# Kernel tuning notes

Measured on AMD Instinct MI355X. Metric: run time of the kernel, lower is better.

The kernel has to match this reference:

```python
import jax, jax.numpy as jnp
import numpy as np

B, T, C, H = 2, 2048, 1024, 16
DH = C // H  # head_size = 64
EPS = 1e-5


def layernorm_axis1(x, gamma, beta):
    # Faithful to the torch code: mean/var over dim 1 (TIME axis), unbiased var.
    mean = jnp.mean(x, axis=1, keepdims=True)
    var = jnp.var(x, axis=1, ddof=1, keepdims=True)
    xhat = (x - mean) / jnp.sqrt(var + EPS)
    return gamma * xhat + beta


def setup_inputs() -> dict:
    key = jax.random.key(0)
    ks = jax.random.split(key, 16)
    s_in = 1.0 / np.sqrt(C)
    s_cat = 1.0 / np.sqrt(H * DH)
    s_ff = 1.0 / np.sqrt(4 * C)
    return {
        "x": jax.random.normal(ks[0], (B, T, C), dtype=jnp.float32),
        # per-head Q/K/V projections (no bias), stacked: [H, C, DH]
        "Wq": jax.random.uniform(ks[1], (H, C, DH), jnp.float32, -s_in, s_in),
        "Wk": jax.random.uniform(ks[2], (H, C, DH), jnp.float32, -s_in, s_in),
        "Wv": jax.random.uniform(ks[3], (H, C, DH), jnp.float32, -s_in, s_in),
        # attention output projection [H*DH, C] + bias
        "Wo": jax.random.uniform(ks[4], (H * DH, C), jnp.float32, -s_cat, s_cat),
        "bo": jax.random.uniform(ks[5], (C,), jnp.float32, -s_cat, s_cat),
        # FFN
        "W1": jax.random.uniform(ks[6], (C, 4 * C), jnp.float32, -s_in, s_in),
        "b1": jax.random.uniform(ks[7], (4 * C,), jnp.float32, -s_in, s_in),
        "W2": jax.random.uniform(ks[8], (4 * C, C), jnp.float32, -s_ff, s_ff),
        "b2": jax.random.uniform(ks[9], (C,), jnp.float32, -s_ff, s_ff),
        # LayerNorm affine params (plain tensors in the original)
        "gamma1": jnp.ones((C,), jnp.float32),
        "beta1": jnp.zeros((C,), jnp.float32),
        "gamma2": jnp.ones((C,), jnp.float32),
        "beta2": jnp.zeros((C,), jnp.float32),
    }


def reference(x, Wq, Wk, Wv, Wo, bo, W1, b1, W2, b2, gamma1, beta1, gamma2, beta2):
    # --- pre-LN attention sublayer ---
    x1 = layernorm_axis1(x, gamma1, beta1)                     # [B,T,C]
    q = jnp.einsum("btc,hcd->bhtd", x1, Wq)                    # [B,H,T,DH]
    k = jnp.einsum("btc,hcd->bhtd", x1, Wk)
    v = jnp.einsum("btc,hcd->bhtd", x1, Wv)
    # NOTE: scaled by full embedding dim C (not head_size) — faithful to source.
    scores = jnp.einsum("bhtd,bhsd->bhts", q, k) * (C ** -0.5)  # [B,H,T,T]
    causal = jnp.tril(jnp.ones((T, T), dtype=bool))
    scores = jnp.where(causal, scores, -jnp.inf)
    wei = jax.nn.softmax(scores, axis=-1)
    attn = jnp.einsum("bhts,bhsd->bhtd", wei, v)               # [B,H,T,DH]
    attn = attn.transpose(0, 2, 1, 3).reshape(B, T, H * DH)    # concat heads
    x = x + attn @ Wo + bo
    # --- pre-LN FFN sublayer ---
    x2 = layernorm_axis1(x, gamma2, beta2)
    h = jax.nn.relu(x2 @ W1 + b1)
    x = x + h @ W2 + b2
    return x
```

## Files before the change

kernel.cpp:

```cpp
#include <hip/hip_runtime.h>
#include <math.h>


#define TDIM 2048
#define BDIM 2
#define CDIM 1024
#define HDIM 16
#define DHE  64
#define QKVS 3072
#define NT   32
#define LNEPS 1e-5f
#define SC2  0.0450842200278f

typedef float f32x4 __attribute__((ext_vector_type(4)));
typedef __bf16 bf16x8 __attribute__((ext_vector_type(8)));
typedef __bf16 bf16x4 __attribute__((ext_vector_type(4)));

__device__ __forceinline__ void gld_lds16(const __bf16* g, __bf16* l) {
  __builtin_amdgcn_global_load_lds(
      (const __attribute__((address_space(1))) void*)g,
      (__attribute__((address_space(3))) void*)l, 16, 0, 0);
}

__global__ __launch_bounds__(256) void ln_stats(const float* __restrict__ x,
                                                float* __restrict__ sumv,
                                                float* __restrict__ sqv) {
  int c = blockIdx.x * 256 + threadIdx.x;
  int b = blockIdx.y;
  int t0 = blockIdx.z * (TDIM / 16);
  const float* xp = x + ((size_t)b * TDIM + t0) * CDIM + c;
  float s = 0.f, q = 0.f;
  for (int t = 0; t < TDIM / 16; ++t) {
    float v = xp[(size_t)t * CDIM];
    s += v;
    q += v * v;
  }
  atomicAdd(&sumv[b * CDIM + c], s);
  atomicAdd(&sqv[b * CDIM + c], q);
}

__global__ __launch_bounds__(256) void ln_apply(const float* __restrict__ x,
    const float* __restrict__ sumv, const float* __restrict__ sqv,
    const float* __restrict__ gamma, const float* __restrict__ beta,
    __bf16* __restrict__ y) {
  size_t i = (size_t)blockIdx.x * 256 + threadIdx.x;
  int c = (int)(i & (CDIM - 1));
  int b = (int)(i >> 21);
  float mean = sumv[b * CDIM + c] * (1.f / TDIM);
  float var = (sqv[b * CDIM + c] - mean * mean * (float)TDIM) * (1.f / (TDIM - 1));
  float rstd = rsqrtf(var + LNEPS);
  y[i] = (__bf16)(gamma[c] * (x[i] - mean) * rstd + beta[c]);
}

__global__ __launch_bounds__(256) void pack_all(
    const float* __restrict__ Wq, const float* __restrict__ Wk,
    const float* __restrict__ Wv, const float* __restrict__ Wo,
    const float* __restrict__ W1, const float* __restrict__ W2,
    __bf16* __restrict__ Wqkvb, __bf16* __restrict__ Wob,
    __bf16* __restrict__ W1b, __bf16* __restrict__ W2b) {
  __shared__ float tile[32][33];
  int t = blockIdx.x;
  int tx = threadIdx.x & 31, ty = threadIdx.x >> 5;
  if (t < 3072) {
    int mat = t >> 10, rem = t & 1023;
    int h = rem >> 6, rr = rem & 63;
    int c0 = (rr & 31) * 32, d0 = (rr >> 5) * 32;
    const float* W = (mat == 0) ? Wq : (mat == 1) ? Wk : Wv;
#pragma unroll
    for (int i = 0; i < 4; ++i)
      tile[ty + i * 8][tx] = W[((size_t)h * CDIM + c0 + ty + i * 8) * DHE + d0 + tx];
    __syncthreads();
#pragma unroll
    for (int i = 0; i < 4; ++i) {
      int n = mat * 1024 + h * 64 + d0 + ty + i * 8;
      Wqkvb[(size_t)n * CDIM + c0 + tx] = (__bf16)tile[tx][ty + i * 8];
    }
  } else {
    const float* in; __bf16* outp; int Cc, R, l;
    if (t < 4096)      { in = Wo; outp = Wob; R = 1024; Cc = 1024; l = t - 3072; }
    else if (t < 8192) { in = W1; outp = W1b; R = 1024; Cc = 4096; l = t - 4096; }
    else               { in = W2; outp = W2b; R = 4096; Cc = 1024; l = t - 8192; }
    int ncx = Cc >> 5;
    int c0 = (l % ncx) * 32, r0 = (l / ncx) * 32;
#pragma unroll
    for (int i = 0; i < 4; ++i)
      tile[ty + i * 8][tx] = in[(size_t)(r0 + ty + i * 8) * Cc + c0 + tx];
    __syncthreads();
#pragma unroll
    for (int i = 0; i < 4; ++i)
      outp[(size_t)(c0 + ty + i * 8) * R + r0 + tx] = (__bf16)tile[tx][ty + i * 8];
  }
}

__global__ __launch_bounds__(256) void transp_v(const __bf16* __restrict__ qkv,
    __bf16* __restrict__ vtb) {
  __shared__ __bf16 tile[32][33];
  int bh = blockIdx.y >> 1, d0 = (blockIdx.y & 1) * 32;
  int b = bh >> 4, h = bh & 15;
  int t0 = blockIdx.x * 32;
  int tx = threadIdx.x & 31, ty = threadIdx.x >> 5;
#pragma unroll
  for (int i = 0; i < 4; ++i)
    tile[ty + i * 8][tx] = qkv[((size_t)b * TDIM + t0 + ty + i * 8) * QKVS + 2048 + h * DHE + d0 + tx];
  __syncthreads();
#pragma unroll
  for (int i = 0; i < 4; ++i)
    vtb[((size_t)bh * 64 + d0 + ty + i * 8) * TDIM + t0 + tx] = tile[tx][ty + i * 8];
}

template<bool BIAS, bool RES, bool RELU, bool OUTBF>
__global__ __launch_bounds__(256) void gemm_bf16(
    const __bf16* __restrict__ Ag, const __bf16* __restrict__ Bg,
    const float* __restrict__ bias, const float* __restrict__ res,
    void* __restrict__ Cm, int M, int N, int K) {
  __shared__ __bf16 As[128 * 32];
  __shared__ __bf16 Bs[128 * 32];
  int tid = threadIdx.x;
  int lane = tid & 63, wid = tid >> 6;
  int wr = wid >> 1, wc = wid & 1;
  int m0 = blockIdx.y * 128, n0 = blockIdx.x * 128;
  int srow = tid >> 2, scol = (tid & 3) * 8;
  int l15 = lane & 15, k8 = (lane >> 4) * 8;

  f32x4 acc[4][4];
#pragma unroll
  for (int m = 0; m < 4; ++m)
#pragma unroll
    for (int n = 0; n < 4; ++n) acc[m][n] = (f32x4){0.f, 0.f, 0.f, 0.f};

  for (int k0 = 0; k0 < K; k0 += 32) {
    __syncthreads();
    gld_lds16(Ag + (size_t)(m0 + srow) * K + k0 + scol,       As + tid * 8);
    gld_lds16(Ag + (size_t)(m0 + 64 + srow) * K + k0 + scol,  As + 2048 + tid * 8);
    gld_lds16(Bg + (size_t)(n0 + srow) * K + k0 + scol,       Bs + tid * 8);
    gld_lds16(Bg + (size_t)(n0 + 64 + srow) * K + k0 + scol,  Bs + 2048 + tid * 8);
    __syncthreads();

    bf16x8 af[4], bf[4];
#pragma unroll
    for (int m = 0; m < 4; ++m)
      af[m] = *(const bf16x8*)(As + (wr * 64 + m * 16 + l15) * 32 + k8);
#pragma unroll
    for (int n = 0; n < 4; ++n)
      bf[n] = *(const bf16x8*)(Bs + (wc * 64 + n * 16 + l15) * 32 + k8);
#pragma unroll
    for (int m = 0; m < 4; ++m)
#pragma unroll
      for (int n = 0; n < 4; ++n)
        acc[m][n] = __builtin_amdgcn_mfma_f32_16x16x32_bf16(af[m], bf[n], acc[m][n], 0, 0, 0);
  }

  int rbase = (lane >> 4) * 4;
#pragma unroll
  for (int m = 0; m < 4; ++m) {
    int row = m0 + wr * 64 + m * 16 + rbase;
#pragma unroll
    for (int n = 0; n < 4; ++n) {
      int col = n0 + wc * 64 + n * 16 + l15;
#pragma unroll
      for (int j = 0; j < 4; ++j) {
        float v = acc[m][n][j];
        size_t off = (size_t)(row + j) * N + col;
        if (BIAS) v += bias[col];
        if (RES)  v += res[off];
        if (RELU) v = fmaxf(v, 0.f);
        if (OUTBF) ((__bf16*)Cm)[off] = (__bf16)v;
        else       ((float*)Cm)[off] = v;
      }
    }
  }
}

template<bool BIAS, bool RELU, bool OUTBF>
__global__ __launch_bounds__(512, 2) void gemm256(
    const __bf16* __restrict__ Ag, const __bf16* __restrict__ Bg,
    const float* __restrict__ bias, void* __restrict__ Cm, void* __restrict__ Cm2,
    int M, int N, int K, int ld, int gnx) {
  __shared__ __align__(16) char lds[131072];
  int tid = threadIdx.x;
  int lane = tid & 63, wid = tid >> 6;
  int wm = wid >> 2, wn = wid & 3;
  int l15 = lane & 15, hi = lane >> 4;

  size_t koff = (size_t)blockIdx.y * K;
  Ag += koff; Bg += koff;
  void* Cuse = blockIdx.y ? Cm2 : Cm;

  int nwg = gridDim.x;
  int q = nwg >> 3, r = nwg & 7;
  int xcd = blockIdx.x & 7, pos = blockIdx.x >> 3;
  int wgid = (xcd < r ? xcd * (q + 1) : r * (q + 1) + (xcd - r) * q) + pos;
  int m0 = (wgid / gnx) * 256, n0 = (wgid % gnx) * 256;

  int sr = tid >> 3;
  int skcol = ((tid & 7) ^ (sr & 7)) << 3;

  const int ac0 = (hi * 16) ^ ((l15 & 7) << 4);
  const int ac1 = ac0 ^ 64;

  f32x4 acc[8][4];
#pragma unroll
  for (int i = 0; i < 8; ++i)
#pragma unroll
    for (int j = 0; j < 4; ++j) acc[i][j] = (f32x4){0.f, 0.f, 0.f, 0.f};

  auto stage = [&](const __bf16* __restrict__ G, int grow0, int k0, char* dst) {
#pragma unroll
    for (int c = 0; c < 2; ++c)
      gld_lds16(G + (size_t)(grow0 + c * 64 + sr) * ld + k0 + skcol,
                (__bf16*)(dst + c * 8192) + (size_t)tid * 8);
  };

  int KT = K >> 6;
  stage(Ag, m0,       0, lds);
  stage(Ag, m0 + 128, 0, lds + 16384);
  stage(Bg, n0,       0, lds + 32768);
  stage(Bg, n0 + 128, 0, lds + 32768 + 16384);
  asm volatile("s_waitcnt vmcnt(0)" ::: "memory");
  __builtin_amdgcn_s_barrier();

  bf16x8 a[4][2], b[4][2];

#define LOADA(MH) do { \
    const char* Ac_ = lds + (size_t)cur * 65536; \
    int rb_ = (wm * 128 + (MH) * 64 + l15) * 128; \
    _Pragma("unroll") \
    for (int i_ = 0; i_ < 4; ++i_) { \
      a[i_][0] = *(const bf16x8*)(Ac_ + rb_ + i_ * 2048 + ac0); \
      a[i_][1] = *(const bf16x8*)(Ac_ + rb_ + i_ * 2048 + ac1); \
    } } while (0)
#define LOADBF do { \
    const char* Bc_ = lds + (size_t)cur * 65536 + 32768; \
    int rb_ = (wn * 64 + l15) * 128; \
    _Pragma("unroll") \
    for (int j_ = 0; j_ < 4; ++j_) { \
      b[j_][0] = *(const bf16x8*)(Bc_ + rb_ + j_ * 2048 + ac0); \
      b[j_][1] = *(const bf16x8*)(Bc_ + rb_ + j_ * 2048 + ac1); \
    } } while (0)
#define QUAD(MH, NH) do { \
    _Pragma("unroll") \
    for (int i_ = 0; i_ < 4; ++i_) \
    _Pragma("unroll") \
    for (int j_ = 0; j_ < 2; ++j_) { \
      acc[(MH)*4+i_][(NH)*2+j_] = __builtin_amdgcn_mfma_f32_16x16x32_bf16( \
          a[i_][0], b[(NH)*2+j_][0], acc[(MH)*4+i_][(NH)*2+j_], 0, 0, 0); \
      acc[(MH)*4+i_][(NH)*2+j_] = __builtin_amdgcn_mfma_f32_16x16x32_bf16( \
          a[i_][1], b[(NH)*2+j_][1], acc[(MH)*4+i_][(NH)*2+j_], 0, 0, 0); \
    } } while (0)

  for (int kt = 0; kt < KT; ++kt) {
    int cur = kt & 1;
    char* Lnxt = lds + (size_t)(cur ^ 1) * 65536;
    int k1 = (kt + 1) << 6;
    if (kt < KT - 1) {
      stage(Ag, m0,       k1, Lnxt);
      stage(Ag, m0 + 128, k1, Lnxt + 16384);
      stage(Bg, n0,       k1, Lnxt + 32768);
      stage(Bg, n0 + 128, k1, Lnxt + 32768 + 16384);
    }
    LOADBF;
    LOADA(0);
    __builtin_amdgcn_s_setprio(1);
    QUAD(0, 0); QUAD(0, 1);
    __builtin_amdgcn_s_setprio(0);
    LOADA(1);
    __builtin_amdgcn_s_setprio(1);
    QUAD(1, 0); QUAD(1, 1);
    __builtin_amdgcn_s_setprio(0);
    asm volatile("" ::: "memory");
    asm volatile("s_waitcnt vmcnt(0)" ::: "memory");
    __builtin_amdgcn_s_barrier();
  }
#undef LOADA
#undef LOADBF
#undef QUAD

#pragma unroll
  for (int fm = 0; fm < 8; ++fm) {
    int row = m0 + wm * 128 + fm * 16 + hi * 4;
#pragma unroll
    for (int fn = 0; fn < 4; ++fn) {
      int col = n0 + wn * 64 + fn * 16 + l15;
#pragma unroll
      for (int j = 0; j < 4; ++j) {
        float v = acc[fm][fn][j];
        size_t off = (size_t)(row + j) * N + col;
        if (BIAS) v += bias[col];
        if (RELU) v = fmaxf(v, 0.f);
        if (OUTBF) ((__bf16*)Cuse)[off] = (__bf16)v;
        else       ((float*)Cuse)[off] = v;
      }
    }
  }
}

__global__ __launch_bounds__(256) void ffn2_reduce(const float* __restrict__ p0,
    const float* __restrict__ p1, const float* __restrict__ b2,
    const float* __restrict__ xmid, float* __restrict__ out) {
  size_t i = ((size_t)blockIdx.x * 256 + threadIdx.x) * 4;
  int c = (int)(i & (CDIM - 1));
  float4 a = *(const float4*)(p0 + i);
  float4 b = *(const float4*)(p1 + i);
  float4 r = *(const float4*)(xmid + i);
  float4 bb = *(const float4*)(b2 + c);
  float4 v;
  v.x = a.x + b.x + r.x + bb.x;
  v.y = a.y + b.y + r.y + bb.y;
  v.z = a.z + b.z + r.z + bb.z;
  v.w = a.w + b.w + r.w + bb.w;
  *(float4*)(out + i) = v;
}

__global__ __launch_bounds__(512, 4) void attn_mfma(const __bf16* __restrict__ qkv,
    const __bf16* __restrict__ vt, __bf16* __restrict__ o) {
  __shared__ __align__(16) char smem[55296];
  __bf16 (*Ks)[64][72] = (__bf16 (*)[64][72])(smem);
  __bf16 (*Vs)[64][72] = (__bf16 (*)[64][72])(smem + 18432);
  __bf16 (*Ps)[16][72] = (__bf16 (*)[16][72])(smem + 36864);
  float (*Os)[64]      = (float (*)[64])(smem);
  float* ms = (float*)(smem + 16384);
  float* ls = (float*)(smem + 16640);

  int bh = blockIdx.y;
  int b = bh >> 4, h = bh & 15;
  int bxA = blockIdx.x;
  int bxB = NT - 1 - bxA;
  int tid = threadIdx.x;
  int lane = tid & 63, w = tid >> 6;
  int wq = w & 3;
  int g = w >> 2;
  int l15 = lane & 15, hi = lane >> 4;
  int hi4 = hi * 4;
  size_t bT = (size_t)b * TDIM;

  bf16x8 onesb;
#pragma unroll
  for (int i = 0; i < 8; ++i) onesb[i] = (l15 == 0) ? (__bf16)1.0f : (__bf16)0.0f;

  bf16x8 qfA[2], qfB[2];
  {
    const __bf16* qp = qkv + (bT + bxA * 64 + wq * 16 + l15) * QKVS + h * DHE;
    qfA[0] = *(const bf16x8*)(qp + hi * 8);
    qfA[1] = *(const bf16x8*)(qp + 32 + hi * 8);
    qp = qkv + (bT + bxB * 64 + wq * 16 + l15) * QKVS + h * DHE;
    qfB[0] = *(const bf16x8*)(qp + hi * 8);
    qfB[1] = *(const bf16x8*)(qp + 32 + hi * 8);
  }

  float mA = -INFINITY, mB = -INFINITY;
  f32x4 lA = (f32x4){0.f, 0.f, 0.f, 0.f};
  f32x4 lB = (f32x4){0.f, 0.f, 0.f, 0.f};
  f32x4 oA[4], oB[4];
#pragma unroll
  for (int n = 0; n < 4; ++n) {
    oA[n] = (f32x4){0.f, 0.f, 0.f, 0.f};
    oB[n] = (f32x4){0.f, 0.f, 0.f, 0.f};
  }

  int g_tid = tid & 255;
  int r0 = g_tid >> 3, c8 = (g_tid & 7) * 8;

  auto process = [&](const bf16x8* qf, float& m_i, f32x4& l_acc, f32x4* oacc,
                     int bx, int t2) {
    f32x4 sacc[4];
#pragma unroll
    for (int n = 0; n < 4; ++n) sacc[n] = (f32x4){0.f, 0.f, 0.f, 0.f};
    __builtin_amdgcn_s_setprio(1);
#pragma unroll
    for (int n = 0; n < 4; ++n)
#pragma unroll
      for (int kk = 0; kk < 2; ++kk) {
        bf16x8 kf = *(const bf16x8*)&Ks[g][n * 16 + l15][kk * 32 + hi * 8];
        sacc[n] = __builtin_amdgcn_mfma_f32_16x16x32_bf16(kf, qf[kk], sacc[n], 0, 0, 0);
      }
    __builtin_amdgcn_s_setprio(0);

    int myq = wq * 16 + l15;
    if (t2 == bx) {
#pragma unroll
      for (int n = 0; n < 4; ++n)
#pragma unroll
        for (int j = 0; j < 4; ++j)
          if (n * 16 + hi4 + j > myq) sacc[n][j] = -INFINITY;
    }

    float mx = sacc[0][0];
#pragma unroll
    for (int n = 0; n < 4; ++n) {
      float a0 = fmaxf(sacc[n][0], sacc[n][1]);
      float a1 = fmaxf(sacc[n][2], sacc[n][3]);
      mx = fmaxf(mx, fmaxf(a0, a1));
    }
    mx = fmaxf(mx, __shfl_xor(mx, 16));
    mx = fmaxf(mx, __shfl_xor(mx, 32));
    mx *= SC2;

    if (!__all(mx - m_i <= 8.0f)) {
      float nm = fmaxf(m_i, mx);
      float al = exp2f(m_i - nm);
      m_i = nm;
#pragma unroll
      for (int r = 0; r < 4; ++r) {
        float ao = __shfl(al, hi4 + r);
        l_acc[r] *= ao;
#pragma unroll
        for (int n = 0; n < 4; ++n) oacc[n][r] *= ao;
      }
    }

    float negm = -m_i;
#pragma unroll
    for (int n = 0; n < 4; ++n) {
      bf16x4 pv;
#pragma unroll
      for (int j = 0; j < 4; ++j)
        pv[j] = (__bf16)exp2f(fmaf(sacc[n][j], SC2, negm));
      *(bf16x4*)&Ps[w][l15][n * 16 + hi4] = pv;
    }

    bf16x8 pa0 = *(const bf16x8*)&Ps[w][l15][hi * 8];
    bf16x8 pa1 = *(const bf16x8*)&Ps[w][l15][32 + hi * 8];
    __builtin_amdgcn_s_setprio(1);
#pragma unroll
    for (int n = 0; n < 4; ++n) {
      bf16x8 vf0 = *(const bf16x8*)&Vs[g][n * 16 + l15][hi * 8];
      bf16x8 vf1 = *(const bf16x8*)&Vs[g][n * 16 + l15][32 + hi * 8];
      oacc[n] = __builtin_amdgcn_mfma_f32_16x16x32_bf16(pa0, vf0, oacc[n], 0, 0, 0);
      oacc[n] = __builtin_amdgcn_mfma_f32_16x16x32_bf16(pa1, vf1, oacc[n], 0, 0, 0);
    }
    l_acc = __builtin_amdgcn_mfma_f32_16x16x32_bf16(pa0, onesb, l_acc, 0, 0, 0);
    l_acc = __builtin_amdgcn_mfma_f32_16x16x32_bf16(pa1, onesb, l_acc, 0, 0, 0);
    __builtin_amdgcn_s_setprio(0);
  };

  for (int j = 0; j <= bxB / 2; ++j) {
    int t2 = 2 * j + g;
    bool have = (t2 <= bxB);
    __syncthreads();
    if (have) {
#pragma unroll
      for (int rr = 0; rr < 2; ++rr) {
        int row = rr * 32 + r0;
        *(bf16x8*)&Ks[g][row][c8] =
            *(const bf16x8*)(qkv + (bT + t2 * 64 + row) * QKVS + 1024 + h * DHE + c8);
        *(bf16x8*)&Vs[g][row][c8] =
            *(const bf16x8*)(vt + ((size_t)bh * 64 + row) * TDIM + t2 * 64 + c8);
      }
    }
    __syncthreads();
    if (t2 <= bxA) process(qfA, mA, lA, oA, bxA, t2);
    if (have)      process(qfB, mB, lB, oB, bxB, t2);
  }

  auto merge = [&](int bx, float m_i, const f32x4& l_acc, f32x4* oacc) {
    float m_o[4], l_o[4];
#pragma unroll
    for (int r = 0; r < 4; ++r) {
      m_o[r] = __shfl(m_i, hi4 + r);
      l_o[r] = __shfl(l_acc[r], lane & 48);
    }
    __syncthreads();
    if (g == 1) {
#pragma unroll
      for (int r = 0; r < 4; ++r) {
        int lrow = wq * 16 + hi4 + r;
        if (l15 == 0) { ms[lrow] = m_o[r]; ls[lrow] = l_o[r]; }
#pragma unroll
        for (int n = 0; n < 4; ++n)
          Os[lrow][n * 16 + l15] = oacc[n][r];
      }
    }
    __syncthreads();
    if (g == 0) {
#pragma unroll
      for (int r = 0; r < 4; ++r) {
        int lrow = wq * 16 + hi4 + r;
        float m1 = ms[lrow], l1 = ls[lrow];
        float mm = fmaxf(m_o[r], m1);
        float e0 = exp2f(m_o[r] - mm), e1 = exp2f(m1 - mm);
        float inv = 1.f / (l_o[r] * e0 + l1 * e1);
        size_t row = bT + bx * 64 + lrow;
#pragma unroll
        for (int n = 0; n < 4; ++n) {
          float v = (oacc[n][r] * e0 + Os[lrow][n * 16 + l15] * e1) * inv;
          o[row * CDIM + h * DHE + n * 16 + l15] = (__bf16)v;
        }
      }
    }
  };
  merge(bxA, mA, lA, oA);
  merge(bxB, mB, lB, oB);
}

extern "C" void kernel_launch(void* const* d_in, const int* in_sizes, int n_in,
                              void* d_out, int out_size, void* d_ws, size_t ws_size,
                              hipStream_t stream) {
  (void)in_sizes; (void)n_in; (void)out_size; (void)ws_size;
  const float* x   = (const float*)d_in[0];
  const float* Wq  = (const float*)d_in[1];
  const float* Wk  = (const float*)d_in[2];
  const float* Wv  = (const float*)d_in[3];
  const float* Wo  = (const float*)d_in[4];
  const float* bo  = (const float*)d_in[5];
  const float* W1  = (const float*)d_in[6];
  const float* b1  = (const float*)d_in[7];
  const float* W2  = (const float*)d_in[8];
  const float* b2  = (const float*)d_in[9];
  const float* g1  = (const float*)d_in[10];
  const float* be1 = (const float*)d_in[11];
  const float* g2  = (const float*)d_in[12];
  const float* be2 = (const float*)d_in[13];
  float* out = (float*)d_out;

  char* wsb = (char*)d_ws;
  const size_t MB = 1024 * 1024;
  __bf16* Wqkvb = (__bf16*)(wsb + 0);
  __bf16* Wob   = (__bf16*)(wsb + 6  * MB);
  __bf16* W1b   = (__bf16*)(wsb + 8  * MB);
  __bf16* W2b   = (__bf16*)(wsb + 16 * MB);
  __bf16* qkvb  = (__bf16*)(wsb + 24 * MB);
  __bf16* hb    = (__bf16*)(wsb + 24 * MB);
  __bf16* vtb   = (__bf16*)(wsb + 48 * MB);
  __bf16* x1b   = (__bf16*)(wsb + 56 * MB);
  __bf16* attnb = (__bf16*)(wsb + 56 * MB);
  float*  xmid  = (float*) (wsb + 64 * MB);
  __bf16* x2b   = (__bf16*)(wsb + 80 * MB);
  float*  stats = (float*) (wsb + 88 * MB);
  float*  p0    = (float*) (wsb + 0);
  float*  p1    = (float*) (wsb + 48 * MB);
  float* sum1 = stats,        *sq1 = stats + 2048;
  float* sum2 = stats + 4096, *sq2 = stats + 6144;

  hipMemsetAsync(stats, 0, 4 * 2048 * sizeof(float), stream);

  pack_all<<<dim3(12288), 256, 0, stream>>>(Wq, Wk, Wv, Wo, W1, W2,
                                            Wqkvb, Wob, W1b, W2b);

  ln_stats<<<dim3(CDIM / 256, BDIM, 16), 256, 0, stream>>>(x, sum1, sq1);
  ln_apply<<<dim3((BDIM * TDIM * CDIM) / 256), 256, 0, stream>>>(x, sum1, sq1, g1, be1, x1b);

  gemm256<false, false, true><<<dim3(192, 1), 512, 0, stream>>>(
      x1b, Wqkvb, nullptr, qkvb, qkvb, 4096, 3072, 1024, 1024, 12);

  transp_v<<<dim3(TDIM / 32, 64), 256, 0, stream>>>(qkvb, vtb);

  attn_mfma<<<dim3(NT / 2, BDIM * HDIM), 512, 0, stream>>>(qkvb, vtb, attnb);

  gemm_bf16<true, true, false, false><<<dim3(8, 32), 256, 0, stream>>>(
      attnb, Wob, bo, x, xmid, 4096, 1024, 1024);

  ln_stats<<<dim3(CDIM / 256, BDIM, 16), 256, 0, stream>>>(xmid, sum2, sq2);
  ln_apply<<<dim3((BDIM * TDIM * CDIM) / 256), 256, 0, stream>>>(xmid, sum2, sq2, g2, be2, x2b);

  gemm256<true, true, true><<<dim3(256, 1), 512, 0, stream>>>(
      x2b, W1b, b1, hb, hb, 4096, 4096, 1024, 1024, 16);

  gemm256<false, false, false><<<dim3(64, 2), 512, 0, stream>>>(
      hb, W2b, nullptr, p0, p1, 4096, 1024, 2048, 4096, 4);
  ffn2_reduce<<<dim3(4096), 256, 0, stream>>>(p0, p1, b2, xmid, out);
}
```

Baseline: 257.3 us.

## Rework gemm256 into four-stage K=32 pipeline and split-K the output projection

The big GEMM kernel now stages 32-wide K slices into a four-buffer LDS ring with three tiles in flight, using partial vmcnt waits in place of a full drain each iteration. The LDS swizzle is changed to match the narrower 64-byte rows. The attention output projection moves from the small 128x128 GEMM to gemm256 with a two-way split-K, followed by a shared reduction kernel that adds bias and residual. This aims to hide global load latency and raise MFMA utilisation, at the cost of more barriers per K step and an extra reduction pass with fp32 partial traffic.

```diff
diff --git a/kernel.cpp b/kernel.cpp
--- a/kernel.cpp
+++ b/kernel.cpp
@@ -108,69 +108,6 @@
     vtb[((size_t)bh * 64 + d0 + ty + i * 8) * TDIM + t0 + tx] = tile[tx][ty + i * 8];
 }
 
-template<bool BIAS, bool RES, bool RELU, bool OUTBF>
-__global__ __launch_bounds__(256) void gemm_bf16(
-    const __bf16* __restrict__ Ag, const __bf16* __restrict__ Bg,
-    const float* __restrict__ bias, const float* __restrict__ res,
-    void* __restrict__ Cm, int M, int N, int K) {
-  __shared__ __bf16 As[128 * 32];
-  __shared__ __bf16 Bs[128 * 32];
-  int tid = threadIdx.x;
-  int lane = tid & 63, wid = tid >> 6;
-  int wr = wid >> 1, wc = wid & 1;
-  int m0 = blockIdx.y * 128, n0 = blockIdx.x * 128;
-  int srow = tid >> 2, scol = (tid & 3) * 8;
-  int l15 = lane & 15, k8 = (lane >> 4) * 8;
-
-  f32x4 acc[4][4];
-#pragma unroll
-  for (int m = 0; m < 4; ++m)
-#pragma unroll
-    for (int n = 0; n < 4; ++n) acc[m][n] = (f32x4){0.f, 0.f, 0.f, 0.f};
-
-  for (int k0 = 0; k0 < K; k0 += 32) {
-    __syncthreads();
-    gld_lds16(Ag + (size_t)(m0 + srow) * K + k0 + scol,       As + tid * 8);
-    gld_lds16(Ag + (size_t)(m0 + 64 + srow) * K + k0 + scol,  As + 2048 + tid * 8);
-    gld_lds16(Bg + (size_t)(n0 + srow) * K + k0 + scol,       Bs + tid * 8);
-    gld_lds16(Bg + (size_t)(n0 + 64 + srow) * K + k0 + scol,  Bs + 2048 + tid * 8);
-    __syncthreads();
-
-    bf16x8 af[4], bf[4];
-#pragma unroll
-    for (int m = 0; m < 4; ++m)
-      af[m] = *(const bf16x8*)(As + (wr * 64 + m * 16 + l15) * 32 + k8);
-#pragma unroll
-    for (int n = 0; n < 4; ++n)
-      bf[n] = *(const bf16x8*)(Bs + (wc * 64 + n * 16 + l15) * 32 + k8);
-#pragma unroll
-    for (int m = 0; m < 4; ++m)
-#pragma unroll
-      for (int n = 0; n < 4; ++n)
-        acc[m][n] = __builtin_amdgcn_mfma_f32_16x16x32_bf16(af[m], bf[n], acc[m][n], 0, 0, 0);
-  }
-
-  int rbase = (lane >> 4) * 4;
-#pragma unroll
-  for (int m = 0; m < 4; ++m) {
-    int row = m0 + wr * 64 + m * 16 + rbase;
-#pragma unroll
-    for (int n = 0; n < 4; ++n) {
-      int col = n0 + wc * 64 + n * 16 + l15;
-#pragma unroll
-      for (int j = 0; j < 4; ++j) {
-        float v = acc[m][n][j];
-        size_t off = (size_t)(row + j) * N + col;
-        if (BIAS) v += bias[col];
-        if (RES)  v += res[off];
-        if (RELU) v = fmaxf(v, 0.f);
-        if (OUTBF) ((__bf16*)Cm)[off] = (__bf16)v;
-        else       ((float*)Cm)[off] = v;
-      }
-    }
-  }
-}
-
 template<bool BIAS, bool RELU, bool OUTBF>
 __global__ __launch_bounds__(512, 2) void gemm256(
     const __bf16* __restrict__ Ag, const __bf16* __restrict__ Bg,
@@ -192,11 +129,9 @@
   int wgid = (xcd < r ? xcd * (q + 1) : r * (q + 1) + (xcd - r) * q) + pos;
   int m0 = (wgid / gnx) * 256, n0 = (wgid % gnx) * 256;
 
-  int sr = tid >> 3;
-  int skcol = ((tid & 7) ^ (sr & 7)) << 3;
-
-  const int ac0 = (hi * 16) ^ ((l15 & 7) << 4);
-  const int ac1 = ac0 ^ 64;
+  int srow = tid >> 2;
+  int skcol = ((tid & 3) ^ ((tid >> 4) & 3)) << 3;
+  const int acS = ((hi ^ ((l15 >> 2) & 3)) << 4);
 
   f32x4 acc[8][4];
 #pragma unroll
@@ -204,76 +139,48 @@
 #pragma unroll
     for (int j = 0; j < 4; ++j) acc[i][j] = (f32x4){0.f, 0.f, 0.f, 0.f};
 
-  auto stage = [&](const __bf16* __restrict__ G, int grow0, int k0, char* dst) {
+  auto stageM = [&](const __bf16* __restrict__ G, int grow0, int k0, char* dst) {
 #pragma unroll
     for (int c = 0; c < 2; ++c)
-      gld_lds16(G + (size_t)(grow0 + c * 64 + sr) * ld + k0 + skcol,
+      gld_lds16(G + (size_t)(grow0 + c * 128 + srow) * ld + k0 + skcol,
                 (__bf16*)(dst + c * 8192) + (size_t)tid * 8);
   };
-
-  int KT = K >> 6;
-  stage(Ag, m0,       0, lds);
-  stage(Ag, m0 + 128, 0, lds + 16384);
-  stage(Bg, n0,       0, lds + 32768);
-  stage(Bg, n0 + 128, 0, lds + 32768 + 16384);
-  asm volatile("s_waitcnt vmcnt(0)" ::: "memory");
+  auto stageT = [&](int t) {
+    char* dst = lds + (size_t)(t & 3) * 32768;
+    stageM(Ag, m0, t << 5, dst);
+    stageM(Bg, n0, t << 5, dst + 16384);
+  };
+
+  int KT = K >> 5;
+  stageT(0); stageT(1); stageT(2);
+  asm volatile("s_waitcnt vmcnt(8)" ::: "memory");
   __builtin_amdgcn_s_barrier();
 
-  bf16x8 a[4][2], b[4][2];
-
-#define LOADA(MH) do { \
-    const char* Ac_ = lds + (size_t)cur * 65536; \
-    int rb_ = (wm * 128 + (MH) * 64 + l15) * 128; \
-    _Pragma("unroll") \
-    for (int i_ = 0; i_ < 4; ++i_) { \
-      a[i_][0] = *(const bf16x8*)(Ac_ + rb_ + i_ * 2048 + ac0); \
-      a[i_][1] = *(const bf16x8*)(Ac_ + rb_ + i_ * 2048 + ac1); \
-    } } while (0)
-#define LOADBF do { \
-    const char* Bc_ = lds + (size_t)cur * 65536 + 32768; \
-    int rb_ = (wn * 64 + l15) * 128; \
-    _Pragma("unroll") \
-    for (int j_ = 0; j_ < 4; ++j_) { \
-      b[j_][0] = *(const bf16x8*)(Bc_ + rb_ + j_ * 2048 + ac0); \
-      b[j_][1] = *(const bf16x8*)(Bc_ + rb_ + j_ * 2048 + ac1); \
-    } } while (0)
-#define QUAD(MH, NH) do { \
-    _Pragma("unroll") \
-    for (int i_ = 0; i_ < 4; ++i_) \
-    _Pragma("unroll") \
-    for (int j_ = 0; j_ < 2; ++j_) { \
-      acc[(MH)*4+i_][(NH)*2+j_] = __builtin_amdgcn_mfma_f32_16x16x32_bf16( \
-          a[i_][0], b[(NH)*2+j_][0], acc[(MH)*4+i_][(NH)*2+j_], 0, 0, 0); \
-      acc[(MH)*4+i_][(NH)*2+j_] = __builtin_amdgcn_mfma_f32_16x16x32_bf16( \
-          a[i_][1], b[(NH)*2+j_][1], acc[(MH)*4+i_][(NH)*2+j_], 0, 0, 0); \
-    } } while (0)
-
-  for (int kt = 0; kt < KT; ++kt) {
-    int cur = kt & 1;
-    char* Lnxt = lds + (size_t)(cur ^ 1) * 65536;
-    int k1 = (kt + 1) << 6;
-    if (kt < KT - 1) {
-      stage(Ag, m0,       k1, Lnxt);
-      stage(Ag, m0 + 128, k1, Lnxt + 16384);
-      stage(Bg, n0,       k1, Lnxt + 32768);
-      stage(Bg, n0 + 128, k1, Lnxt + 32768 + 16384);
-    }
-    LOADBF;
-    LOADA(0);
+  bf16x8 a[8], b[4];
+  for (int t = 0; t < KT; ++t) {
+    if (t + 3 < KT) stageT(t + 3);
+    const char* buf = lds + (size_t)(t & 3) * 32768;
+#pragma unroll
+    for (int i = 0; i < 8; ++i)
+      a[i] = *(const bf16x8*)(buf + (wm * 128 + i * 16 + l15) * 64 + acS);
+#pragma unroll
+    for (int j = 0; j < 4; ++j)
+      b[j] = *(const bf16x8*)(buf + 16384 + (wn * 64 + j * 16 + l15) * 64 + acS);
     __builtin_amdgcn_s_setprio(1);
-    QUAD(0, 0); QUAD(0, 1);
+#pragma unroll
+    for (int i = 0; i < 8; ++i)
+#pragma unroll
+      for (int j = 0; j < 4; ++j)
+        acc[i][j] = __builtin_amdgcn_mfma_f32_16x16x32_bf16(a[i], b[j], acc[i][j], 0, 0, 0);
     __builtin_amdgcn_s_setprio(0);
-    LOADA(1);
-    __builtin_amdgcn_s_setprio(1);
-    QUAD(1, 0); QUAD(1, 1);
-    __builtin_amdgcn_s_setprio(0);
-    asm volatile("" ::: "memory");
-    asm volatile("s_waitcnt vmcnt(0)" ::: "memory");
-    __builtin_amdgcn_s_barrier();
-  }
-#undef LOADA
-#undef LOADBF
-#undef QUAD
+    if (t + 1 < KT) {
+      asm volatile("" ::: "memory");
+      if (t + 3 < KT)      asm volatile("s_waitcnt vmcnt(8)" ::: "memory");
+      else if (t + 2 < KT) asm volatile("s_waitcnt vmcnt(4)" ::: "memory");
+      else                 asm volatile("s_waitcnt vmcnt(0)" ::: "memory");
+      __builtin_amdgcn_s_barrier();
+    }
+  }
 
 #pragma unroll
   for (int fm = 0; fm < 8; ++fm) {
@@ -294,15 +201,15 @@
   }
 }
 
-__global__ __launch_bounds__(256) void ffn2_reduce(const float* __restrict__ p0,
-    const float* __restrict__ p1, const float* __restrict__ b2,
-    const float* __restrict__ xmid, float* __restrict__ out) {
+__global__ __launch_bounds__(256) void splitk_reduce(const float* __restrict__ p0,
+    const float* __restrict__ p1, const float* __restrict__ bias,
+    const float* __restrict__ res, float* __restrict__ out) {
   size_t i = ((size_t)blockIdx.x * 256 + threadIdx.x) * 4;
   int c = (int)(i & (CDIM - 1));
   float4 a = *(const float4*)(p0 + i);
   float4 b = *(const float4*)(p1 + i);
-  float4 r = *(const float4*)(xmid + i);
-  float4 bb = *(const float4*)(b2 + c);
+  float4 r = *(const float4*)(res + i);
+  float4 bb = *(const float4*)(bias + c);
   float4 v;
   v.x = a.x + b.x + r.x + bb.x;
   v.y = a.y + b.y + r.y + bb.y;
@@ -526,6 +433,8 @@
   float*  xmid  = (float*) (wsb + 64 * MB);
   __bf16* x2b   = (__bf16*)(wsb + 80 * MB);
   float*  stats = (float*) (wsb + 88 * MB);
+  float*  q0    = (float*) (wsb + 24 * MB);
+  float*  q1    = (float*) (wsb + 40 * MB);
   float*  p0    = (float*) (wsb + 0);
   float*  p1    = (float*) (wsb + 48 * MB);
   float* sum1 = stats,        *sq1 = stats + 2048;
@@ -546,8 +455,9 @@
 
   attn_mfma<<<dim3(NT / 2, BDIM * HDIM), 512, 0, stream>>>(qkvb, vtb, attnb);
 
-  gemm_bf16<true, true, false, false><<<dim3(8, 32), 256, 0, stream>>>(
-      attnb, Wob, bo, x, xmid, 4096, 1024, 1024);
+  gemm256<false, false, false><<<dim3(64, 2), 512, 0, stream>>>(
+      attnb, Wob, nullptr, q0, q1, 4096, 1024, 512, 1024, 4);
+  splitk_reduce<<<dim3(4096), 256, 0, stream>>>(q0, q1, bo, x, xmid);
 
   ln_stats<<<dim3(CDIM / 256, BDIM, 16), 256, 0, stream>>>(xmid, sum2, sq2);
   ln_apply<<<dim3((BDIM * TDIM * CDIM) / 256), 256, 0, stream>>>(xmid, sum2, sq2, g2, be2, x2b);
@@ -557,5 +467,5 @@
 
   gemm256<false, false, false><<<dim3(64, 2), 512, 0, stream>>>(
       hb, W2b, nullptr, p0, p1, 4096, 1024, 2048, 4096, 4);
-  ffn2_reduce<<<dim3(4096), 256, 0, stream>>>(p0, p1, b2, xmid, out);
-}
+  splitk_reduce<<<dim3(4096), 256, 0, stream>>>(p0, p1, b2, xmid, out);
+}
```

Result: slower. 282.5 us (+9.8%).

## Run attention output projection on 256-tile split-K GEMM with fused reduce

Applied to the files above, without the earlier changes.

Drops the small 128x128 gemm_bf16 kernel. The attention output projection now runs on the 256x256 gemm256 kernel with a 2-way split-K, followed by a reduce kernel that adds the bias and the residual. The reduce kernel is generalised to take split output pointers so the partial buffers can be placed in freed workspace regions, and the workspace layout is reshuffled to fit. The XCD-aware workgroup remapping in gemm256 is also removed for all GEMMs, which may change L2 locality. The split-K adds an extra fp32 partial-sum round trip through memory.

```diff
diff --git a/kernel.cpp b/kernel.cpp
--- a/kernel.cpp
+++ b/kernel.cpp
@@ -108,73 +108,11 @@
     vtb[((size_t)bh * 64 + d0 + ty + i * 8) * TDIM + t0 + tx] = tile[tx][ty + i * 8];
 }
 
-template<bool BIAS, bool RES, bool RELU, bool OUTBF>
-__global__ __launch_bounds__(256) void gemm_bf16(
-    const __bf16* __restrict__ Ag, const __bf16* __restrict__ Bg,
-    const float* __restrict__ bias, const float* __restrict__ res,
-    void* __restrict__ Cm, int M, int N, int K) {
-  __shared__ __bf16 As[128 * 32];
-  __shared__ __bf16 Bs[128 * 32];
-  int tid = threadIdx.x;
-  int lane = tid & 63, wid = tid >> 6;
-  int wr = wid >> 1, wc = wid & 1;
-  int m0 = blockIdx.y * 128, n0 = blockIdx.x * 128;
-  int srow = tid >> 2, scol = (tid & 3) * 8;
-  int l15 = lane & 15, k8 = (lane >> 4) * 8;
-
-  f32x4 acc[4][4];
-#pragma unroll
-  for (int m = 0; m < 4; ++m)
-#pragma unroll
-    for (int n = 0; n < 4; ++n) acc[m][n] = (f32x4){0.f, 0.f, 0.f, 0.f};
-
-  for (int k0 = 0; k0 < K; k0 += 32) {
-    __syncthreads();
-    gld_lds16(Ag + (size_t)(m0 + srow) * K + k0 + scol,       As + tid * 8);
-    gld_lds16(Ag + (size_t)(m0 + 64 + srow) * K + k0 + scol,  As + 2048 + tid * 8);
-    gld_lds16(Bg + (size_t)(n0 + srow) * K + k0 + scol,       Bs + tid * 8);
-    gld_lds16(Bg + (size_t)(n0 + 64 + srow) * K + k0 + scol,  Bs + 2048 + tid * 8);
-    __syncthreads();
-
-    bf16x8 af[4], bf[4];
-#pragma unroll
-    for (int m = 0; m < 4; ++m)
-      af[m] = *(const bf16x8*)(As + (wr * 64 + m * 16 + l15) * 32 + k8);
-#pragma unroll
-    for (int n = 0; n < 4; ++n)
-      bf[n] = *(const bf16x8*)(Bs + (wc * 64 + n * 16 + l15) * 32 + k8);
-#pragma unroll
-    for (int m = 0; m < 4; ++m)
-#pragma unroll
-      for (int n = 0; n < 4; ++n)
-        acc[m][n] = __builtin_amdgcn_mfma_f32_16x16x32_bf16(af[m], bf[n], acc[m][n], 0, 0, 0);
-  }
-
-  int rbase = (lane >> 4) * 4;
-#pragma unroll
-  for (int m = 0; m < 4; ++m) {
-    int row = m0 + wr * 64 + m * 16 + rbase;
-#pragma unroll
-    for (int n = 0; n < 4; ++n) {
-      int col = n0 + wc * 64 + n * 16 + l15;
-#pragma unroll
-      for (int j = 0; j < 4; ++j) {
-        float v = acc[m][n][j];
-        size_t off = (size_t)(row + j) * N + col;
-        if (BIAS) v += bias[col];
-        if (RES)  v += res[off];
-        if (RELU) v = fmaxf(v, 0.f);
-        if (OUTBF) ((__bf16*)Cm)[off] = (__bf16)v;
-        else       ((float*)Cm)[off] = v;
-      }
-    }
-  }
-}
-
 template<bool BIAS, bool RELU, bool OUTBF>
 __global__ __launch_bounds__(512, 2) void gemm256(
     const __bf16* __restrict__ Ag, const __bf16* __restrict__ Bg,
-    const float* __restrict__ bias, void* __restrict__ Cm, void* __restrict__ Cm2,
+    const float* __restrict__ bias, void* __restrict__ Cm,
+    void* __restrict__ Cm2, void* __restrict__ Cm3, int msplit,
     int M, int N, int K, int ld, int gnx) {
   __shared__ __align__(16) char lds[131072];
   int tid = threadIdx.x;
@@ -184,17 +122,14 @@
 
   size_t koff = (size_t)blockIdx.y * K;
   Ag += koff; Bg += koff;
-  void* Cuse = blockIdx.y ? Cm2 : Cm;
-
-  int nwg = gridDim.x;
-  int q = nwg >> 3, r = nwg & 7;
-  int xcd = blockIdx.x & 7, pos = blockIdx.x >> 3;
-  int wgid = (xcd < r ? xcd * (q + 1) : r * (q + 1) + (xcd - r) * q) + pos;
+
+  int wgid = blockIdx.x;
   int m0 = (wgid / gnx) * 256, n0 = (wgid % gnx) * 256;
+
+  void* Cuse = blockIdx.y ? (m0 < msplit ? Cm2 : Cm3) : Cm;
 
   int sr = tid >> 3;
   int skcol = ((tid & 7) ^ (sr & 7)) << 3;
-
   const int ac0 = (hi * 16) ^ ((l15 & 7) << 4);
   const int ac1 = ac0 ^ 64;
 
@@ -294,15 +229,18 @@
   }
 }
 
-__global__ __launch_bounds__(256) void ffn2_reduce(const float* __restrict__ p0,
-    const float* __restrict__ p1, const float* __restrict__ b2,
-    const float* __restrict__ xmid, float* __restrict__ out) {
+__global__ __launch_bounds__(256) void splitk_reduce(const float* __restrict__ p0,
+    const float* __restrict__ p1a, const float* __restrict__ p1b, int msplit,
+    const float* __restrict__ bias, const float* __restrict__ res,
+    float* __restrict__ out) {
   size_t i = ((size_t)blockIdx.x * 256 + threadIdx.x) * 4;
   int c = (int)(i & (CDIM - 1));
+  int row = (int)(i >> 10);
+  const float* p1 = (row < msplit) ? p1a : p1b;
   float4 a = *(const float4*)(p0 + i);
   float4 b = *(const float4*)(p1 + i);
-  float4 r = *(const float4*)(xmid + i);
-  float4 bb = *(const float4*)(b2 + c);
+  float4 r = *(const float4*)(res + i);
+  float4 bb = *(const float4*)(bias + c);
   float4 v;
   v.x = a.x + b.x + r.x + bb.x;
   v.y = a.y + b.y + r.y + bb.y;
@@ -526,8 +464,11 @@
   float*  xmid  = (float*) (wsb + 64 * MB);
   __bf16* x2b   = (__bf16*)(wsb + 80 * MB);
   float*  stats = (float*) (wsb + 88 * MB);
+  float*  q0    = (float*) (wsb + 24 * MB);
+  float*  q1    = (float*) (wsb + 40 * MB);
   float*  p0    = (float*) (wsb + 0);
-  float*  p1    = (float*) (wsb + 48 * MB);
+  float*  p1a   = (float*) (wsb + 56 * MB);
+  float*  p1b   = (float*) (wsb + 80 * MB) - 2048 * 1024;
   float* sum1 = stats,        *sq1 = stats + 2048;
   float* sum2 = stats + 4096, *sq2 = stats + 6144;
 
@@ -540,22 +481,23 @@
   ln_apply<<<dim3((BDIM * TDIM * CDIM) / 256), 256, 0, stream>>>(x, sum1, sq1, g1, be1, x1b);
 
   gemm256<false, false, true><<<dim3(192, 1), 512, 0, stream>>>(
-      x1b, Wqkvb, nullptr, qkvb, qkvb, 4096, 3072, 1024, 1024, 12);
+      x1b, Wqkvb, nullptr, qkvb, qkvb, qkvb, 0, 4096, 3072, 1024, 1024, 12);
 
   transp_v<<<dim3(TDIM / 32, 64), 256, 0, stream>>>(qkvb, vtb);
 
   attn_mfma<<<dim3(NT / 2, BDIM * HDIM), 512, 0, stream>>>(qkvb, vtb, attnb);
 
-  gemm_bf16<true, true, false, false><<<dim3(8, 32), 256, 0, stream>>>(
-      attnb, Wob, bo, x, xmid, 4096, 1024, 1024);
+  gemm256<false, false, false><<<dim3(64, 2), 512, 0, stream>>>(
+      attnb, Wob, nullptr, q0, q1, q1, 4096, 4096, 1024, 512, 1024, 4);
+  splitk_reduce<<<dim3(4096), 256, 0, stream>>>(q0, q1, q1, 4096, bo, x, xmid);
 
   ln_stats<<<dim3(CDIM / 256, BDIM, 16), 256, 0, stream>>>(xmid, sum2, sq2);
   ln_apply<<<dim3((BDIM * TDIM * CDIM) / 256), 256, 0, stream>>>(xmid, sum2, sq2, g2, be2, x2b);
 
   gemm256<true, true, true><<<dim3(256, 1), 512, 0, stream>>>(
-      x2b, W1b, b1, hb, hb, 4096, 4096, 1024, 1024, 16);
+      x2b, W1b, b1, hb, hb, hb, 0, 4096, 4096, 1024, 1024, 16);
 
   gemm256<false, false, false><<<dim3(64, 2), 512, 0, stream>>>(
-      hb, W2b, nullptr, p0, p1, 4096, 1024, 2048, 4096, 4);
-  ffn2_reduce<<<dim3(4096), 256, 0, stream>>>(p0, p1, b2, xmid, out);
-}
+      hb, W2b, nullptr, p0, p1a, p1b, 2048, 4096, 1024, 2048, 4096, 4);
+  splitk_reduce<<<dim3(4096), 256, 0, stream>>>(p0, p1a, p1b, 2048, b2, xmid, out);
+}
```

After: 260.5 us. Within noise of the previous version (+1.2%).
